# Optimization experiments

Measured on AMD Instinct MI355X. Metric: run time of the kernel, lower is better.

The kernel has to match this reference:

```python
import jax, jax.numpy as jnp
import numpy as np

B, T, C, H = 4, 2048, 1024, 16
D = C // H  # head_dim = 64


def setup_inputs() -> dict:
    key = jax.random.key(0)
    k1, k2, k3, k4 = jax.random.split(key, 4)
    x = jax.random.normal(k1, (B, T, C), dtype=jnp.float32)
    # realistic padding: each sequence has length in [T//2, T]
    lengths = jax.random.randint(k4, (B,), T // 2, T + 1)
    padding_mask = jnp.arange(T)[None, :] < lengths[:, None]  # True = keep
    # weights stored [in, out] (equivalent to torch Linear weight transposed)
    w_qkv = jax.random.normal(k2, (C, 3 * C), dtype=jnp.float32) * (C ** -0.5)
    w_out = jax.random.normal(k3, (C, C), dtype=jnp.float32) * (C ** -0.5)
    b_out = jnp.zeros((C,), dtype=jnp.float32)
    return {"x": x, "padding_mask": padding_mask, "w_qkv": w_qkv, "w_out": w_out, "b_out": b_out}


def reference(x, padding_mask, w_qkv, w_out, b_out):
    scale = D ** -0.5
    qkv = x @ w_qkv  # [B,T,3C]
    q, k, v = jnp.split(qkv, 3, axis=-1)

    def split_heads(t):
        return t.reshape(B, T, H, D).transpose(0, 2, 1, 3)  # [B,H,T,D]

    q, k, v = split_heads(q), split_heads(k), split_heads(v)
    attn = jnp.einsum("bhqd,bhkd->bhqk", q, k) * scale  # [B,H,T,T]
    mask = padding_mask[:, None, None, :]  # [B,1,1,T]
    attn = jnp.where(mask, attn, jnp.finfo(attn.dtype).min)
    attn = jax.nn.softmax(attn, axis=-1)
    # dropout is identity in eval mode
    out = jnp.einsum("bhqk,bhkd->bhqd", attn, v)  # [B,H,T,D]
    out = out.transpose(0, 2, 1, 3).reshape(B, T, C)
    return out @ w_out + b_out
```

## Files before the change

### kernel.cpp

```cpp
#include <hip/hip_runtime.h>
#include <hip/hip_bf16.h>

#define Bb 4
#define Tt 2048
#define Cc 1024
#define Hh 16

typedef unsigned short u16;
typedef __attribute__((ext_vector_type(8))) __bf16 bf16x8;
typedef __attribute__((ext_vector_type(4))) float  f32x4;

__device__ __forceinline__ u16 f2bf_hw(float f) {
    __bf16 h = (__bf16)f;
    return *(u16*)&h;
}

__device__ __forceinline__ unsigned cvt_pk_bf16(float a, float b) {
    unsigned r;
    asm("v_cvt_pk_bf16_f32 %0, %1, %2" : "=v"(r) : "v"(a), "v"(b));
    return r;
}

__device__ __forceinline__ float fexp2(float x) {
#if __has_builtin(__builtin_amdgcn_exp2f)
    return __builtin_amdgcn_exp2f(x);
#else
    return __expf(x * 0.6931471805599453f);
#endif
}

__device__ __forceinline__ void gld_lds16(const void* g, void* l) {
    __builtin_amdgcn_global_load_lds(
        (__attribute__((address_space(1))) void*)(g),
        (__attribute__((address_space(3))) void*)(l),
        16, 0, 0);
}

__device__ __forceinline__ f32x4 mfma16(bf16x8 a, bf16x8 b, f32x4 c) {
    return __builtin_amdgcn_mfma_f32_16x16x32_bf16(a, b, c, 0, 0, 0);
}

__global__ void cast_f32_bf16(const float* __restrict__ in, u16* __restrict__ out, int n4) {
    int i = blockIdx.x * 256 + threadIdx.x;
    if (i < n4) {
        float4 v = ((const float4*)in)[i];
        uint2 o;
        o.x = cvt_pk_bf16(v.x, v.y);
        o.y = cvt_pk_bf16(v.z, v.w);
        ((uint2*)out)[i] = o;
    }
}

__global__ void castT_f32_bf16(const float* __restrict__ in, u16* __restrict__ out,
                               int K, int N, int scaleN, float sv) {
    __shared__ float Ls[64][65];
    const int n0 = blockIdx.x * 64, k0 = blockIdx.y * 64;
    const int t = threadIdx.x;
    #pragma unroll
    for (int s = 0; s < 4; ++s) {
        int idx = t + 256 * s;
        int r   = idx >> 4;
        int c4  = (idx & 15) * 4;
        float4 v = *(const float4*)&in[(size_t)(k0 + r) * N + n0 + c4];
        Ls[r][c4 + 0] = v.x; Ls[r][c4 + 1] = v.y;
        Ls[r][c4 + 2] = v.z; Ls[r][c4 + 3] = v.w;
    }
    __syncthreads();
    #pragma unroll
    for (int s = 0; s < 2; ++s) {
        int idx = t + 256 * s;
        int n   = idx >> 3;
        int kc  = (idx & 7) * 8;
        const float sc = (n0 + n < scaleN) ? sv : 1.0f;
        alignas(16) u16 tmp[8];
        #pragma unroll
        for (int i = 0; i < 8; ++i) tmp[i] = f2bf_hw(Ls[kc + i][n] * sc);
        *(uint4*)&out[(size_t)(n0 + n) * K + k0 + kc] = *(const uint4*)tmp;
    }
}

__global__ void repack_frags(const u16* __restrict__ qkv,
                             u16* __restrict__ kx, u16* __restrict__ vx) {
    __shared__ u16 Kt[64 * 80];
    __shared__ u16 Vt[64 * 80];
    const int t = threadIdx.x;
    const int ch = blockIdx.x, bh = blockIdx.y, b = bh >> 4, h = bh & 15;
    const int kc = ch * 64;

    #pragma unroll
    for (int u = 0; u < 2; ++u) {
        int id = t + 256 * u;
        int key = id >> 3, c8 = id & 7;
        const size_t row = (size_t)(b * Tt + kc + key) * (3 * Cc) + h * 64 + c8 * 8;
        *(uint4*)&Kt[key * 80 + c8 * 8] = *(const uint4*)&qkv[row + Cc];
        *(uint4*)&Vt[key * 80 + c8 * 8] = *(const uint4*)&qkv[row + 2 * Cc];
    }
    __syncthreads();

    const size_t obase = (size_t)(bh * 32 + ch) * 4096;
    #pragma unroll
    for (int u = 0; u < 2; ++u) {
        int id = t + 256 * u;
        int lane = id & 63, ks = (id >> 6) & 1, jt = id >> 7;
        int l16 = lane & 15, quad = lane >> 4;
        uint4 kv = *(const uint4*)&Kt[(16 * jt + l16) * 80 + 32 * ks + quad * 8];
        *(uint4*)&kx[obase + (size_t)(jt * 2 + ks) * 512 + lane * 8] = kv;
        alignas(16) u16 tmp[8];
        #pragma unroll
        for (int j = 0; j < 8; ++j)
            tmp[j] = Vt[(32 * ks + quad * 8 + j) * 80 + 16 * jt + l16];
        *(uint4*)&vx[obase + (size_t)(jt * 2 + ks) * 512 + lane * 8] = *(const uint4*)tmp;
    }
}

__global__ __launch_bounds__(256, 3) void gemm_bt_bf16(
    const u16* __restrict__ A, const u16* __restrict__ Bt,
    const float* __restrict__ bias,
    u16* __restrict__ outB, float* __restrict__ outF,
    int M, int N, int K)
{
    __shared__ u16 As[128 * 32];
    __shared__ u16 Bs[128 * 32];
    const int t = threadIdx.x;
    const int w = t >> 6, lane = t & 63;
    const int quad = lane >> 4, l16 = lane & 15;
    const int wr = w >> 1, wc = w & 1;
    const int m0 = blockIdx.y * 128, n0 = blockIdx.x * 128;

    int aoff[4], boff[4];
    #pragma unroll
    for (int i = 0; i < 4; ++i) {
        int rA = 64 * wr + 16 * i + l16;
        aoff[i] = rA * 32 + ((quad ^ ((rA >> 1) & 3)) * 8);
        int rB = 64 * wc + 16 * i + l16;
        boff[i] = rB * 32 + ((quad ^ ((rB >> 1) & 3)) * 8);
    }

    f32x4 acc[4][4] = {};

    for (int k0 = 0; k0 < K; k0 += 32) {
        __syncthreads();
        #pragma unroll
        for (int u = 0; u < 2; ++u) {
            const int i   = 2 * w + u;
            const int row = 16 * i + (lane >> 2);
            const int c   = (lane & 3) ^ ((row >> 1) & 3);
            gld_lds16(A  + (size_t)(m0 + row) * K + k0 + c * 8, (void*)(As + i * 512 + lane * 8));
            gld_lds16(Bt + (size_t)(n0 + row) * K + k0 + c * 8, (void*)(Bs + i * 512 + lane * 8));
        }
        asm volatile("s_waitcnt vmcnt(0)" ::: "memory");
        __syncthreads();

        bf16x8 af[4], bfr[4];
        #pragma unroll
        for (int i = 0; i < 4; ++i) af[i]  = *(const bf16x8*)&As[aoff[i]];
        #pragma unroll
        for (int j = 0; j < 4; ++j) bfr[j] = *(const bf16x8*)&Bs[boff[j]];
        #pragma unroll
        for (int i = 0; i < 4; ++i)
            #pragma unroll
            for (int j = 0; j < 4; ++j)
                acc[i][j] = mfma16(af[i], bfr[j], acc[i][j]);
    }

    const int rbase = m0 + 64 * wr + quad * 4;
    const int cbase = n0 + 64 * wc + l16;
    if (outF) {
        float bv[4];
        #pragma unroll
        for (int j = 0; j < 4; ++j) bv[j] = bias[cbase + 16 * j];
        #pragma unroll
        for (int i = 0; i < 4; ++i)
            #pragma unroll
            for (int r = 0; r < 4; ++r) {
                size_t ro = (size_t)(rbase + 16 * i + r) * N;
                #pragma unroll
                for (int j = 0; j < 4; ++j)
                    outF[ro + cbase + 16 * j] = acc[i][j][r] + bv[j];
            }
    } else {
        #pragma unroll
        for (int i = 0; i < 4; ++i)
            #pragma unroll
            for (int r = 0; r < 4; ++r) {
                size_t ro = (size_t)(rbase + 16 * i + r) * N;
                #pragma unroll
                for (int j = 0; j < 4; ++j)
                    outB[ro + cbase + 16 * j] = f2bf_hw(acc[i][j][r]);
            }
    }
}

__global__ __launch_bounds__(256, 2) void attn_mfma4(
    const u16* __restrict__ qkv, const u16* __restrict__ kx, const u16* __restrict__ vx,
    const int* __restrict__ mask, u16* __restrict__ outO)
{
    __shared__ u16 KVs[2][8192];
    __shared__ u16 Pss[4][64 * 68];

    const int t = threadIdx.x;
    const int w = t >> 6, lane = t & 63;
    const int quad = lane >> 4, l16 = lane & 15;
    const int bh = blockIdx.x, qb = blockIdx.y, b = bh >> 4, h = bh & 15;

    int sum = 0;
    {
        const int4* mp = (const int4*)(mask + b * Tt) + lane * 8;
        #pragma unroll
        for (int i = 0; i < 8; ++i) { int4 m4 = mp[i]; sum += m4.x + m4.y + m4.z + m4.w; }
        #pragma unroll
        for (int off = 1; off < 64; off <<= 1) sum += __shfl_xor(sum, off);
    }
    const int L = sum;

    const int q0 = qb * 256 + w * 64;
    bf16x8 qf[4][2];
    #pragma unroll
    for (int qq = 0; qq < 4; ++qq) {
        const u16* qp = qkv + (size_t)(b * Tt + q0 + 16 * qq + l16) * (3 * Cc) + h * 64 + quad * 8;
        qf[qq][0] = *(const bf16x8*)(qp);
        qf[qq][1] = *(const bf16x8*)(qp + 32);
    }

    f32x4 oacc[4][4] = {};
    f32x4 lacc[4]    = {};
    const __bf16 onebf = (__bf16)1.0f;
    const bf16x8 ones  = {onebf, onebf, onebf, onebf, onebf, onebf, onebf, onebf};

    const int nfull = L >> 6;
    const int nch   = (L + 63) >> 6;
    const size_t cb0 = (size_t)bh * 32 * 4096;
    u16* Pw = Pss[w];

    {
        const u16* ksrc = kx + cb0;
        const u16* vsrc = vx + cb0;
        gld_lds16(ksrc + t * 8,        &KVs[0][t * 8]);
        gld_lds16(ksrc + 2048 + t * 8, &KVs[0][2048 + t * 8]);
        gld_lds16(vsrc + t * 8,        &KVs[0][4096 + t * 8]);
        gld_lds16(vsrc + 2048 + t * 8, &KVs[0][6144 + t * 8]);
    }
    __syncthreads();

    for (int ch = 0; ch < nch; ++ch) {
        const int p = ch & 1;

        {
            const int cc = (ch + 1 < nch) ? ch + 1 : ch;
            const u16* ksrc = kx + cb0 + (size_t)cc * 4096;
            const u16* vsrc = vx + cb0 + (size_t)cc * 4096;
            u16* d = KVs[p ^ 1];
            gld_lds16(ksrc + t * 8,        d + t * 8);
            gld_lds16(ksrc + 2048 + t * 8, d + 2048 + t * 8);
            gld_lds16(vsrc + t * 8,        d + 4096 + t * 8);
            gld_lds16(vsrc + 2048 + t * 8, d + 6144 + t * 8);
        }

        const u16* Kb = KVs[p];
        const u16* Vb = KVs[p] + 4096;

        bf16x8 kf[4][2];
        #pragma unroll
        for (int jt = 0; jt < 4; ++jt)
            #pragma unroll
            for (int ks = 0; ks < 2; ++ks)
                kf[jt][ks] = *(const bf16x8*)&Kb[(jt * 2 + ks) * 512 + lane * 8];

        #pragma unroll
        for (int qq = 0; qq < 4; ++qq) {
            f32x4 st[4];
            #pragma unroll
            for (int jt = 0; jt < 4; ++jt) {
                f32x4 z = {0.f, 0.f, 0.f, 0.f};
                z = mfma16(kf[jt][0], qf[qq][0], z);
                st[jt] = mfma16(kf[jt][1], qf[qq][1], z);
            }
            uint2 pk[4];
            if (ch < nfull) {
                #pragma unroll
                for (int jt = 0; jt < 4; ++jt) {
                    pk[jt].x = cvt_pk_bf16(fexp2(st[jt][0]), fexp2(st[jt][1]));
                    pk[jt].y = cvt_pk_bf16(fexp2(st[jt][2]), fexp2(st[jt][3]));
                }
            } else {
                const int kc = ch * 64;
                #pragma unroll
                for (int jt = 0; jt < 4; ++jt) {
                    const int kb = kc + 16 * jt + quad * 4;
                    float e[4];
                    #pragma unroll
                    for (int r = 0; r < 4; ++r)
                        e[r] = (kb + r < L) ? fexp2(st[jt][r]) : 0.f;
                    pk[jt].x = cvt_pk_bf16(e[0], e[1]);
                    pk[jt].y = cvt_pk_bf16(e[2], e[3]);
                }
            }
            #pragma unroll
            for (int jt = 0; jt < 4; ++jt)
                *(uint2*)&Pw[(16 * qq + l16) * 68 + 16 * jt + quad * 4] = pk[jt];
        }

        bf16x8 vf[4][2];
        #pragma unroll
        for (int dt = 0; dt < 4; ++dt)
            #pragma unroll
            for (int ks = 0; ks < 2; ++ks)
                vf[dt][ks] = *(const bf16x8*)&Vb[(dt * 2 + ks) * 512 + lane * 8];

        #pragma unroll
        for (int qq = 0; qq < 4; ++qq) {
            #pragma unroll
            for (int ks = 0; ks < 2; ++ks) {
                const u16* pr = &Pw[(16 * qq + l16) * 68 + 32 * ks + quad * 8];
                uint2 pa = *(const uint2*)pr;
                uint2 pb = *(const uint2*)(pr + 4);
                uint4 comb = {pa.x, pa.y, pb.x, pb.y};
                bf16x8 pf = *(const bf16x8*)&comb;
                #pragma unroll
                for (int dt = 0; dt < 4; ++dt)
                    oacc[qq][dt] = mfma16(pf, vf[dt][ks], oacc[qq][dt]);
                lacc[qq] = mfma16(pf, ones, lacc[qq]);
            }
        }

        __syncthreads();
    }

    #pragma unroll
    for (int qq = 0; qq < 4; ++qq)
        #pragma unroll
        for (int r = 0; r < 4; ++r) {
            const float inv = 1.f / lacc[qq][r];
            const size_t ro = (size_t)(b * Tt + q0 + 16 * qq + quad * 4 + r) * Cc + h * 64 + l16;
            #pragma unroll
            for (int dt = 0; dt < 4; ++dt)
                outO[ro + 16 * dt] = f2bf_hw(oacc[qq][dt][r] * inv);
        }
}

extern "C" void kernel_launch(void* const* d_in, const int* in_sizes, int n_in,
                              void* d_out, int out_size, void* d_ws, size_t ws_size,
                              hipStream_t stream) {
    const float* x     = (const float*)d_in[0];
    const int*   mask  = (const int*)  d_in[1];
    const float* w_qkv = (const float*)d_in[2];
    const float* w_out = (const float*)d_in[3];
    const float* b_out = (const float*)d_in[4];
    float*       outp  = (float*)d_out;

    const int M = Bb * Tt;
    char* ws = (char*)d_ws;
    u16* xb     = (u16*)(ws);
    u16* wqkvT  = (u16*)(ws + (16u << 20));
    u16* woutT  = (u16*)(ws + (22u << 20));
    u16* qkv    = (u16*)(ws + (24u << 20));
    u16* kx     = (u16*)(ws + (72u << 20));
    u16* vx     = (u16*)(ws + (88u << 20));
    u16* attnO  = (u16*)(ws);

    const float c2 = 0.18033688011112042f;

    cast_f32_bf16<<<(M * Cc / 4 + 255) / 256, 256, 0, stream>>>(x, xb, M * Cc / 4);
    castT_f32_bf16<<<dim3(3 * Cc / 64, Cc / 64), 256, 0, stream>>>(w_qkv, wqkvT, Cc, 3 * Cc, Cc, c2);
    castT_f32_bf16<<<dim3(Cc / 64, Cc / 64), 256, 0, stream>>>(w_out, woutT, Cc, Cc, 0, 1.0f);

    gemm_bt_bf16<<<dim3(3 * Cc / 128, M / 128), 256, 0, stream>>>(
        xb, wqkvT, nullptr, qkv, nullptr, M, 3 * Cc, Cc);

    repack_frags<<<dim3(Tt / 64, Bb * Hh), 256, 0, stream>>>(qkv, kx, vx);

    attn_mfma4<<<dim3(Bb * Hh, Tt / 256), 256, 0, stream>>>(qkv, kx, vx, mask, attnO);

    gemm_bt_bf16<<<dim3(Cc / 128, M / 128), 256, 0, stream>>>(
        attnO, woutT, b_out, nullptr, outp, M, Cc, Cc);
}
```

Measured before the change: 268.5 us.

## Stage K/V prefetch through registers into a single LDS buffer and shrink P scratch

The attention kernel drops the async global-to-LDS double buffer. It now loads the next K/V chunk into registers at the top of each iteration and writes it into a single LDS buffer after a barrier, which adds a second __syncthreads per chunk. The per-wave P scratch shrinks from 64 rows to 16: each 16-row query tile's probabilities are written and then consumed by the PV MFMAs right away. V fragments are also loaded earlier. Together this cuts LDS use to allow more resident blocks, at the cost of extra barriers, more live registers and less overlap of loads with compute.

```diff
diff --git a/kernel.cpp b/kernel.cpp
--- a/kernel.cpp
+++ b/kernel.cpp
@@ -195,8 +195,8 @@
     const u16* __restrict__ qkv, const u16* __restrict__ kx, const u16* __restrict__ vx,
     const int* __restrict__ mask, u16* __restrict__ outO)
 {
-    __shared__ u16 KVs[2][8192];
-    __shared__ u16 Pss[4][64 * 68];
+    __shared__ u16 KVs[8192];
+    __shared__ u16 Pss[4][16 * 68];
 
     const int t = threadIdx.x;
     const int w = t >> 6, lane = t & 63;
@@ -233,31 +233,27 @@
     u16* Pw = Pss[w];
 
     {
-        const u16* ksrc = kx + cb0;
-        const u16* vsrc = vx + cb0;
-        gld_lds16(ksrc + t * 8,        &KVs[0][t * 8]);
-        gld_lds16(ksrc + 2048 + t * 8, &KVs[0][2048 + t * 8]);
-        gld_lds16(vsrc + t * 8,        &KVs[0][4096 + t * 8]);
-        gld_lds16(vsrc + 2048 + t * 8, &KVs[0][6144 + t * 8]);
+        uint4 k0a = *(const uint4*)&kx[cb0 + t * 8];
+        uint4 k0b = *(const uint4*)&kx[cb0 + 2048 + t * 8];
+        uint4 v0a = *(const uint4*)&vx[cb0 + t * 8];
+        uint4 v0b = *(const uint4*)&vx[cb0 + 2048 + t * 8];
+        *(uint4*)&KVs[t * 8]        = k0a;
+        *(uint4*)&KVs[2048 + t * 8] = k0b;
+        *(uint4*)&KVs[4096 + t * 8] = v0a;
+        *(uint4*)&KVs[6144 + t * 8] = v0b;
     }
     __syncthreads();
 
     for (int ch = 0; ch < nch; ++ch) {
-        const int p = ch & 1;
-
-        {
-            const int cc = (ch + 1 < nch) ? ch + 1 : ch;
-            const u16* ksrc = kx + cb0 + (size_t)cc * 4096;
-            const u16* vsrc = vx + cb0 + (size_t)cc * 4096;
-            u16* d = KVs[p ^ 1];
-            gld_lds16(ksrc + t * 8,        d + t * 8);
-            gld_lds16(ksrc + 2048 + t * 8, d + 2048 + t * 8);
-            gld_lds16(vsrc + t * 8,        d + 4096 + t * 8);
-            gld_lds16(vsrc + 2048 + t * 8, d + 6144 + t * 8);
-        }
-
-        const u16* Kb = KVs[p];
-        const u16* Vb = KVs[p] + 4096;
+        const int cc = (ch + 1 < nch) ? ch + 1 : ch;
+        const size_t nb = cb0 + (size_t)cc * 4096;
+        uint4 nk0 = *(const uint4*)&kx[nb + t * 8];
+        uint4 nk1 = *(const uint4*)&kx[nb + 2048 + t * 8];
+        uint4 nv0 = *(const uint4*)&vx[nb + t * 8];
+        uint4 nv1 = *(const uint4*)&vx[nb + 2048 + t * 8];
+
+        const u16* Kb = KVs;
+        const u16* Vb = KVs + 4096;
 
         bf16x8 kf[4][2];
         #pragma unroll
@@ -265,6 +261,13 @@
             #pragma unroll
             for (int ks = 0; ks < 2; ++ks)
                 kf[jt][ks] = *(const bf16x8*)&Kb[(jt * 2 + ks) * 512 + lane * 8];
+
+        bf16x8 vf[4][2];
+        #pragma unroll
+        for (int dt = 0; dt < 4; ++dt)
+            #pragma unroll
+            for (int ks = 0; ks < 2; ++ks)
+                vf[dt][ks] = *(const bf16x8*)&Vb[(dt * 2 + ks) * 512 + lane * 8];
 
         #pragma unroll
         for (int qq = 0; qq < 4; ++qq) {
@@ -297,21 +300,11 @@
             }
             #pragma unroll
             for (int jt = 0; jt < 4; ++jt)
-                *(uint2*)&Pw[(16 * qq + l16) * 68 + 16 * jt + quad * 4] = pk[jt];
-        }
-
-        bf16x8 vf[4][2];
-        #pragma unroll
-        for (int dt = 0; dt < 4; ++dt)
-            #pragma unroll
-            for (int ks = 0; ks < 2; ++ks)
-                vf[dt][ks] = *(const bf16x8*)&Vb[(dt * 2 + ks) * 512 + lane * 8];
-
-        #pragma unroll
-        for (int qq = 0; qq < 4; ++qq) {
+                *(uint2*)&Pw[l16 * 68 + 16 * jt + quad * 4] = pk[jt];
+
             #pragma unroll
             for (int ks = 0; ks < 2; ++ks) {
-                const u16* pr = &Pw[(16 * qq + l16) * 68 + 32 * ks + quad * 8];
+                const u16* pr = &Pw[l16 * 68 + 32 * ks + quad * 8];
                 uint2 pa = *(const uint2*)pr;
                 uint2 pb = *(const uint2*)(pr + 4);
                 uint4 comb = {pa.x, pa.y, pb.x, pb.y};
@@ -323,6 +316,11 @@
             }
         }
 
+        __syncthreads();
+        *(uint4*)&KVs[t * 8]        = nk0;
+        *(uint4*)&KVs[2048 + t * 8] = nk1;
+        *(uint4*)&KVs[4096 + t * 8] = nv0;
+        *(uint4*)&KVs[6144 + t * 8] = nv1;
         __syncthreads();
     }
 
```

Measured after the change: 268.6 us. Within noise of the previous version (+0.0%).
